# Performance work log

Hardware: AMD Instinct MI355X
Metric: run time of the kernel (lower is better)

Reference implementation:

```python
import jax, jax.numpy as jnp
import numpy as np

N_Q, M, D, DV = 4096, 32768, 512, 512  # groups, keys, key dim, value dim


def setup_inputs() -> dict:
    key = jax.random.key(0)
    k1, k2, k3 = jax.random.split(key, 3)
    query = jax.random.normal(k1, (N_Q, D), dtype=jnp.float32)
    keys = jax.random.normal(k2, (M, D), dtype=jnp.float32)
    values = jax.random.normal(k3, (M, DV), dtype=jnp.float32)
    # each query/group owns exactly M//N_Q keys -> no empty softmax rows
    tree_idx = jnp.arange(M, dtype=jnp.int32) % N_Q
    return {"query": query, "keys": keys, "values": values, "tree_idx": tree_idx}


def _l2_normalize(x, eps=1e-12):
    # matches F.normalize(x, dim=1, p=2): x / max(||x||_2, eps)
    n = jnp.linalg.norm(x, axis=1, keepdims=True)
    return x / jnp.maximum(n, eps)


def reference(query, keys, values, tree_idx):
    n_q = query.shape[0]
    # mask[q, m] = (tree_idx[m] == q); equivalent to zeros.index_add(0, tree_idx, eye(M)).bool()
    mask = tree_idx[None, :] == jnp.arange(n_q, dtype=tree_idx.dtype)[:, None]  # [N_q, M]
    query_n = _l2_normalize(query)
    keys_n = _l2_normalize(keys)
    align = query_n @ keys_n.T                      # [N_q, M] cosine similarities
    align = jnp.where(mask, align, -jnp.inf)        # masked_fill_(~mask, -inf)
    alpha = jax.nn.softmax(align, axis=1)           # segment-masked softmax per query
    att = alpha @ values                            # [N_q, DV]
    return att, alpha.sum(axis=0)
```

## Files before the change

kernel.cpp:

```cpp
#include <hip/hip_runtime.h>
#include <math.h>

#define D_DIM 512

__device__ __forceinline__ float d4(const float4& a, const float4& b) {
    return a.x*b.x + a.y*b.y + a.z*b.z + a.w*b.w;
}
__device__ __forceinline__ void fma4(float4& a, float w, const float4& v) {
    a.x += w*v.x; a.y += w*v.y; a.z += w*v.z; a.w += w*v.w;
}

__device__ __forceinline__ void g2l16(const float* g, float* l) {
    __builtin_amdgcn_global_load_lds(
        (const __attribute__((address_space(1))) void*)g,
        (__attribute__((address_space(3))) void*)l, 16, 0, 0);
}

__global__ void k_fill(const int* __restrict__ tree_idx, int m_total, int n_q,
                       int cap, int* __restrict__ cnt, int* __restrict__ keyslot) {
    const int i = blockIdx.x * blockDim.x + threadIdx.x;
    const int base = cnt[n_q];
    if (i < m_total) {
        const int q = tree_idx[i];
        const int old = atomicAdd(&cnt[q], 1);
        const int slot = (int)((unsigned)old - (unsigned)base);
        if (slot >= 0 && slot < cap) keyslot[(size_t)q * cap + slot] = i;
    }
}

__global__ __launch_bounds__(64) void attn_staged(
        const float* __restrict__ query, const float* __restrict__ keys,
        const float* __restrict__ values, const int* __restrict__ cnt,
        const int* __restrict__ keyslot, int cap,
        const int* __restrict__ tree_idx, int m_total,
        float* __restrict__ att, float* __restrict__ colsum, int n_q, int qpb) {
    extern __shared__ float smem[];
    const int lane = threadIdx.x;
    const int q0   = blockIdx.x * qpb;
    const int base = cnt[n_q];

    for (int it = 0; it < qpb; ++it) {
        const int qi = q0 + it;
        if (qi >= n_q) return;
        int nk = (int)((unsigned)cnt[qi] - (unsigned)base);
        if (nk < 0) nk = 0;
        if (nk > cap) nk = cap;
        const size_t off = (size_t)qi * cap;

        const float4* qp = (const float4*)(query + (size_t)qi * D_DIM);
        float4 qa = qp[lane], qb = qp[lane + 64];

        if (nk == 8) {
            int mv = (lane < 8) ? keyslot[off + lane] : 0;
            if (mv < 0 || mv >= m_total) mv = 0;
            int okv = (lane < 8 && tree_idx[mv] == qi) ? 1 : 0;
            int ms[8];
#pragma unroll
            for (int j = 0; j < 8; ++j) ms[j] = __shfl(mv, j);

#pragma unroll
            for (int j = 0; j < 8; ++j) {
                const float* kr = keys   + (size_t)ms[j] * D_DIM;
                const float* vr = values + (size_t)ms[j] * D_DIM;
                g2l16(kr +       (lane << 2), smem + j * 512);
                g2l16(kr + 256 + (lane << 2), smem + j * 512 + 256);
                g2l16(vr +       (lane << 2), smem + 4096 + j * 512);
                g2l16(vr + 256 + (lane << 2), smem + 4096 + j * 512 + 256);
            }
            __syncthreads();

            float pq = d4(qa, qa) + d4(qb, qb);
            float pd[8], pk[8];
#pragma unroll
            for (int j = 0; j < 8; ++j) {
                const float4* kr = (const float4*)(smem + j * 512);
                float4 ka = kr[lane], kb = kr[lane + 64];
                pd[j] = d4(qa, ka) + d4(qb, kb);
                pk[j] = d4(ka, ka) + d4(kb, kb);
            }
#pragma unroll
            for (int o = 32; o > 0; o >>= 1) {
                pq += __shfl_xor(pq, o);
#pragma unroll
                for (int j = 0; j < 8; ++j) {
                    pd[j] += __shfl_xor(pd[j], o);
                    pk[j] += __shfl_xor(pk[j], o);
                }
            }
            const float qinv = 1.0f / fmaxf(sqrtf(pq), 1e-12f);
            float e[8], sum = 0.f;
            int oks[8];
#pragma unroll
            for (int j = 0; j < 8; ++j) {
                oks[j] = __shfl(okv, j);
                e[j] = oks[j] ? __expf(pd[j] * qinv / fmaxf(sqrtf(pk[j]), 1e-12f)) : 0.f;
                sum += e[j];
            }
            const float inv = (sum > 0.f) ? 1.0f / sum : 0.f;

            float4 aa = make_float4(0.f, 0.f, 0.f, 0.f);
            float4 ab = make_float4(0.f, 0.f, 0.f, 0.f);
#pragma unroll
            for (int j = 0; j < 8; ++j) {
                const float4* vr = (const float4*)(smem + 4096 + j * 512);
                float4 va = vr[lane], vb = vr[lane + 64];
                fma4(aa, e[j], va); fma4(ab, e[j], vb);
            }
            aa.x *= inv; aa.y *= inv; aa.z *= inv; aa.w *= inv;
            ab.x *= inv; ab.y *= inv; ab.z *= inv; ab.w *= inv;
            float4* op = (float4*)(att + (size_t)qi * D_DIM);
            op[lane]      = aa;
            op[lane + 64] = ab;
            if (lane == 0) {
#pragma unroll
                for (int j = 0; j < 8; ++j)
                    if (oks[j]) colsum[ms[j]] = e[j] * inv;
            }
            __syncthreads();
        } else {
            float pq = d4(qa, qa) + d4(qb, qb);
#pragma unroll
            for (int o = 32; o > 0; o >>= 1) pq += __shfl_xor(pq, o);
            const float qinv = 1.0f / fmaxf(sqrtf(pq), 1e-12f);
            float sum = 0.f;
            float4 aa = make_float4(0.f, 0.f, 0.f, 0.f);
            float4 ab = make_float4(0.f, 0.f, 0.f, 0.f);
            for (int j = 0; j < nk; ++j) {
                int mi = keyslot[off + j];
                bool ok = (mi >= 0 && mi < m_total && tree_idx[mi] == qi);
                int ci = ok ? mi : 0;
                const float4* kp = (const float4*)(keys   + (size_t)ci * D_DIM);
                const float4* vp = (const float4*)(values + (size_t)ci * D_DIM);
                float4 ka = kp[lane], kb = kp[lane + 64];
                float pd = d4(qa, ka) + d4(qb, kb);
                float pk = d4(ka, ka) + d4(kb, kb);
#pragma unroll
                for (int o = 32; o > 0; o >>= 1) {
                    pd += __shfl_xor(pd, o);
                    pk += __shfl_xor(pk, o);
                }
                float ev = ok ? __expf(pd * qinv / fmaxf(sqrtf(pk), 1e-12f)) : 0.f;
                sum += ev;
                if (lane == 0 && ok) colsum[mi] = ev;
                float4 va = vp[lane], vb = vp[lane + 64];
                fma4(aa, ev, va); fma4(ab, ev, vb);
            }
            const float inv = (sum > 0.f) ? 1.0f / sum : 0.f;
            aa.x *= inv; aa.y *= inv; aa.z *= inv; aa.w *= inv;
            ab.x *= inv; ab.y *= inv; ab.z *= inv; ab.w *= inv;
            float4* op = (float4*)(att + (size_t)qi * D_DIM);
            op[lane]      = aa;
            op[lane + 64] = ab;
            if (lane == 0) {
                for (int j = 0; j < nk; ++j) {
                    int mi = keyslot[off + j];
                    if (mi >= 0 && mi < m_total && tree_idx[mi] == qi)
                        colsum[mi] *= inv;
                }
            }
        }
    }
}

__global__ void k_zero(int* cnt, int n) {
    int i = blockIdx.x * blockDim.x + threadIdx.x;
    if (i < n) cnt[i] = 0;
}
__global__ void k_count(const int* __restrict__ t, int* __restrict__ cnt, int m) {
    int i = blockIdx.x * blockDim.x + threadIdx.x;
    if (i < m) atomicAdd(&cnt[t[i]], 1);
}
__global__ __launch_bounds__(1024) void k_scan(int* __restrict__ cnt,
                                               int* __restrict__ offsets, int n_q) {
    __shared__ int wsum[16];
    const int tid = threadIdx.x, lane = tid & 63, wv = tid >> 6;
    const int items = (n_q + 1023) >> 10;
    const int base = tid * items;
    int local = 0;
    for (int i = 0; i < items; ++i) { int idx = base + i; if (idx < n_q) local += cnt[idx]; }
    int incl = local;
#pragma unroll
    for (int o = 1; o < 64; o <<= 1) { int v = __shfl_up(incl, o); if (lane >= o) incl += v; }
    if (lane == 63) wsum[wv] = incl;
    __syncthreads();
    if (wv == 0) {
        int v = (lane < 16) ? wsum[lane] : 0;
        int iv = v;
#pragma unroll
        for (int o = 1; o < 16; o <<= 1) { int t = __shfl_up(iv, o); if (lane >= o) iv += t; }
        if (lane < 16) wsum[lane] = iv - v;
    }
    __syncthreads();
    int run = wsum[wv] + incl - local;
    for (int i = 0; i < items; ++i) {
        int idx = base + i;
        if (idx < n_q) { int c = cnt[idx]; offsets[idx] = run; cnt[idx] = run; run += c; }
    }
    if (tid == 1023) offsets[n_q] = run;
}
__global__ void k_scatter(const int* __restrict__ t, int* __restrict__ cnt,
                          int* __restrict__ keylist, int m) {
    int i = blockIdx.x * blockDim.x + threadIdx.x;
    if (i < m) { int p = atomicAdd(&cnt[t[i]], 1); keylist[p] = i; }
}
__global__ __launch_bounds__(512, 8) void attn_fb(
        const float* __restrict__ query, const float* __restrict__ keys,
        const float* __restrict__ values, const int* __restrict__ offsets,
        const int* __restrict__ keylist, float* __restrict__ att,
        float* __restrict__ colsum) {
    __shared__ float4 s_v[8][128];
    __shared__ float  s_e[8];
    const int qi = blockIdx.x, tid = threadIdx.x, lane = tid & 63, wv = tid >> 6;
    const int off = offsets[qi];
    const int nk  = offsets[qi + 1] - off;
    const float4* qp = (const float4*)(query + (size_t)qi * D_DIM);
    float4 qa = qp[lane], qb = qp[lane + 64];
    float pq = d4(qa, qa) + d4(qb, qb);
    float4 aa = make_float4(0,0,0,0), ab = make_float4(0,0,0,0);
    float esum = 0.f;
    for (int idx = wv; idx < nk; idx += 8) {
        const int mi = keylist[off + idx];
        const float4* kp = (const float4*)(keys   + (size_t)mi * D_DIM);
        const float4* vp = (const float4*)(values + (size_t)mi * D_DIM);
        float4 ka = kp[lane], kb = kp[lane + 64];
        float4 va = vp[lane], vb = vp[lane + 64];
        float pd = d4(qa, ka) + d4(qb, kb);
        float pk = d4(ka, ka) + d4(kb, kb);
        float pq2 = pq;
#pragma unroll
        for (int o = 32; o > 0; o >>= 1) {
            pd += __shfl_xor(pd, o); pk += __shfl_xor(pk, o); pq2 += __shfl_xor(pq2, o);
        }
        const float qinv = 1.0f / fmaxf(sqrtf(pq2), 1e-12f);
        const float e = __expf(pd * qinv / fmaxf(sqrtf(pk), 1e-12f));
        esum += e;
        if (lane == 0) colsum[mi] = e;
        fma4(aa, e, va); fma4(ab, e, vb);
    }
    if (lane == 0) s_e[wv] = esum;
    s_v[wv][lane] = aa; s_v[wv][64 + lane] = ab;
    __syncthreads();
    const float tot = s_e[0]+s_e[1]+s_e[2]+s_e[3]+s_e[4]+s_e[5]+s_e[6]+s_e[7];
    const float inv = (tot > 0.f) ? 1.0f / tot : 0.f;
    if (tid < 128) {
        float4 r = s_v[0][tid];
#pragma unroll
        for (int j = 1; j < 8; ++j) { float4 p = s_v[j][tid]; r.x+=p.x; r.y+=p.y; r.z+=p.z; r.w+=p.w; }
        r.x *= inv; r.y *= inv; r.z *= inv; r.w *= inv;
        ((float4*)(att + (size_t)qi * D_DIM))[tid] = r;
    }
    if (lane == 0)
        for (int idx = wv; idx < nk; idx += 8) colsum[keylist[off + idx]] *= inv;
}

extern "C" void kernel_launch(void* const* d_in, const int* in_sizes, int n_in,
                              void* d_out, int out_size, void* d_ws, size_t ws_size,
                              hipStream_t stream) {
    const float* query    = (const float*)d_in[0];
    const float* keys     = (const float*)d_in[1];
    const float* values   = (const float*)d_in[2];
    const int*   tree_idx = (const int*)d_in[3];

    const int n_q     = in_sizes[0] / D_DIM;
    const int m_total = in_sizes[3];

    float* att    = (float*)d_out;
    float* colsum = att + (size_t)n_q * D_DIM;

    const long ws_ints = (long)(ws_size / 4);
    long cap_l = (ws_ints - (n_q + 1)) / (n_q > 0 ? n_q : 1);
    if (cap_l > 1024) cap_l = 1024;

    if (cap_l >= 8) {
        const int cap = (int)cap_l;
        int* cnt     = (int*)d_ws;
        int* keyslot = cnt + n_q + 1;
        k_fill<<<(m_total + 255) / 256, 256, 0, stream>>>(tree_idx, m_total, n_q,
                                                          cap, cnt, keyslot);
        int qpb = (n_q + 1023) / 1024;
        if (qpb < 1) qpb = 1;
        int grid = (n_q + qpb - 1) / qpb;
        attn_staged<<<grid, 64, 32768, stream>>>(query, keys, values, cnt,
                                                 keyslot, cap, tree_idx, m_total,
                                                 att, colsum, n_q, qpb);
    } else {
        int* cnt     = (int*)d_ws;
        int* offsets = cnt + n_q;
        int* keylist = offsets + n_q + 1;
        k_zero   <<<(n_q + 255) / 256, 256, 0, stream>>>(cnt, n_q);
        k_count  <<<(m_total + 255) / 256, 256, 0, stream>>>(tree_idx, cnt, m_total);
        k_scan   <<<1, 1024, 0, stream>>>(cnt, offsets, n_q);
        k_scatter<<<(m_total + 255) / 256, 256, 0, stream>>>(tree_idx, cnt, keylist, m_total);
        attn_fb  <<<n_q, 512, 0, stream>>>(query, keys, values, offsets, keylist, att, colsum);
    }
}
```

Before: 170.3 us.

## Add strided slab fast path for round-robin key-to-query assignment

k_fill now counts keys whose group differs from i % n_q. When that count is zero and the shapes fit, the attention kernel skips the keyslot indirection and the per-key tree_idx checks. It instead handles 8 queries per 256-thread block, reading the 8 keys and values of each query at fixed strided row offsets j*n_q+q, with softmax weights shared through LDS. The separate prefix-scan fallback pipeline is removed and replaced by a generic per-wave loop over keyslot. This trades gather indirection and LDS staging for a specialisation that only pays off for one input structure, though the runtime check keeps other inputs correct.

```diff
diff --git a/kernel.cpp b/kernel.cpp
--- a/kernel.cpp
+++ b/kernel.cpp
@@ -2,18 +2,13 @@
 #include <math.h>
 
 #define D_DIM 512
+#define QB 8
 
 __device__ __forceinline__ float d4(const float4& a, const float4& b) {
     return a.x*b.x + a.y*b.y + a.z*b.z + a.w*b.w;
 }
 __device__ __forceinline__ void fma4(float4& a, float w, const float4& v) {
     a.x += w*v.x; a.y += w*v.y; a.z += w*v.z; a.w += w*v.w;
-}
-
-__device__ __forceinline__ void g2l16(const float* g, float* l) {
-    __builtin_amdgcn_global_load_lds(
-        (const __attribute__((address_space(1))) void*)g,
-        (__attribute__((address_space(3))) void*)l, 16, 0, 0);
 }
 
 __global__ void k_fill(const int* __restrict__ tree_idx, int m_total, int n_q,
@@ -22,235 +17,160 @@
     const int base = cnt[n_q];
     if (i < m_total) {
         const int q = tree_idx[i];
-        const int old = atomicAdd(&cnt[q], 1);
-        const int slot = (int)((unsigned)old - (unsigned)base);
-        if (slot >= 0 && slot < cap) keyslot[(size_t)q * cap + slot] = i;
+        if (q < 0 || q >= n_q) {
+            atomicAdd(&cnt[n_q + 1], 1);
+        } else {
+            if (q != (i % n_q)) atomicAdd(&cnt[n_q + 1], 1);
+            const int old = atomicAdd(&cnt[q], 1);
+            const int slot = (int)((unsigned)old - (unsigned)base);
+            if (slot >= 0 && slot < cap) keyslot[(size_t)q * cap + slot] = i;
+        }
     }
 }
 
-__global__ __launch_bounds__(64) void attn_staged(
+__global__ void attn_slab(
         const float* __restrict__ query, const float* __restrict__ keys,
         const float* __restrict__ values, const int* __restrict__ cnt,
         const int* __restrict__ keyslot, int cap,
         const int* __restrict__ tree_idx, int m_total,
-        float* __restrict__ att, float* __restrict__ colsum, int n_q, int qpb) {
-    extern __shared__ float smem[];
-    const int lane = threadIdx.x;
-    const int q0   = blockIdx.x * qpb;
+        float* __restrict__ att, float* __restrict__ colsum,
+        int n_q, int use_slab) {
+    __shared__ float s_pq[QB];
+    __shared__ float s_pd[QB][8];
+    __shared__ float s_pk[QB][8];
+    __shared__ float s_w[QB][8];
+
+    const int q0   = blockIdx.x * QB;
     const int base = cnt[n_q];
-
-    for (int it = 0; it < qpb; ++it) {
-        const int qi = q0 + it;
-        if (qi >= n_q) return;
+    const bool slab = use_slab && (cnt[n_q + 1] == base);
+
+    if (slab) {
+        const int i  = threadIdx.x;
+        const int t  = i >> 5;
+        const int c0 = i & 31;
+        const int qrow = q0 + t;
+
+        const float4* qb = (const float4*)query + (size_t)qrow * 128 + c0;
+        float4 q4[4];
+        float pq = 0.f;
+#pragma unroll
+        for (int r = 0; r < 4; ++r) { q4[r] = qb[r * 32]; pq += d4(q4[r], q4[r]); }
+#pragma unroll
+        for (int o = 1; o < 32; o <<= 1) pq += __shfl_xor(pq, o);
+        if (c0 == 0) s_pq[t] = pq;
+
+#pragma unroll 2
+        for (int j = 0; j < 8; ++j) {
+            const float4* kb = (const float4*)keys
+                             + ((size_t)j * n_q + qrow) * 128 + c0;
+            float pd = 0.f, pk = 0.f;
+#pragma unroll
+            for (int r = 0; r < 4; ++r) {
+                float4 k4 = kb[r * 32];
+                pd += d4(q4[r], k4);
+                pk += d4(k4, k4);
+            }
+#pragma unroll
+            for (int o = 1; o < 32; o <<= 1) {
+                pd += __shfl_xor(pd, o);
+                pk += __shfl_xor(pk, o);
+            }
+            if (c0 == 0) { s_pd[t][j] = pd; s_pk[t][j] = pk; }
+        }
+        __syncthreads();
+
+        if (i < QB) {
+            const float qinv = 1.0f / fmaxf(sqrtf(s_pq[i]), 1e-12f);
+            float e[8], sum = 0.f;
+#pragma unroll
+            for (int j = 0; j < 8; ++j) {
+                e[j] = __expf(s_pd[i][j] * qinv / fmaxf(sqrtf(s_pk[i][j]), 1e-12f));
+                sum += e[j];
+            }
+            const float inv = (sum > 0.f) ? 1.0f / sum : 0.f;
+#pragma unroll
+            for (int j = 0; j < 8; ++j) {
+                const float w = e[j] * inv;
+                s_w[i][j] = w;
+                colsum[(size_t)j * n_q + q0 + i] = w;
+            }
+        }
+        __syncthreads();
+
+        float4 acc[4];
+#pragma unroll
+        for (int r = 0; r < 4; ++r) acc[r] = make_float4(0.f, 0.f, 0.f, 0.f);
+#pragma unroll 2
+        for (int j = 0; j < 8; ++j) {
+            const float w = s_w[t][j];
+            const float4* vb = (const float4*)values
+                             + ((size_t)j * n_q + qrow) * 128 + c0;
+#pragma unroll
+            for (int r = 0; r < 4; ++r) {
+                float4 v4 = vb[r * 32];
+                fma4(acc[r], w, v4);
+            }
+        }
+        float4* ob = (float4*)att + (size_t)qrow * 128 + c0;
+#pragma unroll
+        for (int r = 0; r < 4; ++r) ob[r * 32] = acc[r];
+        return;
+    }
+
+    const int lane = threadIdx.x & 63;
+    const int wv   = threadIdx.x >> 6;
+    for (int u = wv; u < QB; u += 4) {
+        const int qi = q0 + u;
+        if (qi >= n_q) continue;
         int nk = (int)((unsigned)cnt[qi] - (unsigned)base);
         if (nk < 0) nk = 0;
         if (nk > cap) nk = cap;
         const size_t off = (size_t)qi * cap;
 
         const float4* qp = (const float4*)(query + (size_t)qi * D_DIM);
-        float4 qa = qp[lane], qb = qp[lane + 64];
-
-        if (nk == 8) {
-            int mv = (lane < 8) ? keyslot[off + lane] : 0;
-            if (mv < 0 || mv >= m_total) mv = 0;
-            int okv = (lane < 8 && tree_idx[mv] == qi) ? 1 : 0;
-            int ms[8];
-#pragma unroll
-            for (int j = 0; j < 8; ++j) ms[j] = __shfl(mv, j);
-
-#pragma unroll
-            for (int j = 0; j < 8; ++j) {
-                const float* kr = keys   + (size_t)ms[j] * D_DIM;
-                const float* vr = values + (size_t)ms[j] * D_DIM;
-                g2l16(kr +       (lane << 2), smem + j * 512);
-                g2l16(kr + 256 + (lane << 2), smem + j * 512 + 256);
-                g2l16(vr +       (lane << 2), smem + 4096 + j * 512);
-                g2l16(vr + 256 + (lane << 2), smem + 4096 + j * 512 + 256);
-            }
-            __syncthreads();
-
-            float pq = d4(qa, qa) + d4(qb, qb);
-            float pd[8], pk[8];
-#pragma unroll
-            for (int j = 0; j < 8; ++j) {
-                const float4* kr = (const float4*)(smem + j * 512);
-                float4 ka = kr[lane], kb = kr[lane + 64];
-                pd[j] = d4(qa, ka) + d4(qb, kb);
-                pk[j] = d4(ka, ka) + d4(kb, kb);
-            }
+        float4 qa = qp[lane], qb2 = qp[lane + 64];
+        float pq = d4(qa, qa) + d4(qb2, qb2);
+#pragma unroll
+        for (int o = 32; o > 0; o >>= 1) pq += __shfl_xor(pq, o);
+        const float qinv = 1.0f / fmaxf(sqrtf(pq), 1e-12f);
+
+        float sum = 0.f;
+        float4 aa = make_float4(0.f, 0.f, 0.f, 0.f);
+        float4 ab = make_float4(0.f, 0.f, 0.f, 0.f);
+        for (int j = 0; j < nk; ++j) {
+            int mi = keyslot[off + j];
+            bool ok = (mi >= 0 && mi < m_total && tree_idx[mi] == qi);
+            int ci = ok ? mi : 0;
+            const float4* kp = (const float4*)(keys   + (size_t)ci * D_DIM);
+            const float4* vp = (const float4*)(values + (size_t)ci * D_DIM);
+            float4 ka = kp[lane], kb = kp[lane + 64];
+            float pd = d4(qa, ka) + d4(qb2, kb);
+            float pk = d4(ka, ka) + d4(kb, kb);
 #pragma unroll
             for (int o = 32; o > 0; o >>= 1) {
-                pq += __shfl_xor(pq, o);
-#pragma unroll
-                for (int j = 0; j < 8; ++j) {
-                    pd[j] += __shfl_xor(pd[j], o);
-                    pk[j] += __shfl_xor(pk[j], o);
-                }
-            }
-            const float qinv = 1.0f / fmaxf(sqrtf(pq), 1e-12f);
-            float e[8], sum = 0.f;
-            int oks[8];
-#pragma unroll
-            for (int j = 0; j < 8; ++j) {
-                oks[j] = __shfl(okv, j);
-                e[j] = oks[j] ? __expf(pd[j] * qinv / fmaxf(sqrtf(pk[j]), 1e-12f)) : 0.f;
-                sum += e[j];
-            }
-            const float inv = (sum > 0.f) ? 1.0f / sum : 0.f;
-
-            float4 aa = make_float4(0.f, 0.f, 0.f, 0.f);
-            float4 ab = make_float4(0.f, 0.f, 0.f, 0.f);
-#pragma unroll
-            for (int j = 0; j < 8; ++j) {
-                const float4* vr = (const float4*)(smem + 4096 + j * 512);
-                float4 va = vr[lane], vb = vr[lane + 64];
-                fma4(aa, e[j], va); fma4(ab, e[j], vb);
-            }
-            aa.x *= inv; aa.y *= inv; aa.z *= inv; aa.w *= inv;
-            ab.x *= inv; ab.y *= inv; ab.z *= inv; ab.w *= inv;
-            float4* op = (float4*)(att + (size_t)qi * D_DIM);
-            op[lane]      = aa;
-            op[lane + 64] = ab;
-            if (lane == 0) {
-#pragma unroll
-                for (int j = 0; j < 8; ++j)
-                    if (oks[j]) colsum[ms[j]] = e[j] * inv;
-            }
-            __syncthreads();
-        } else {
-            float pq = d4(qa, qa) + d4(qb, qb);
-#pragma unroll
-            for (int o = 32; o > 0; o >>= 1) pq += __shfl_xor(pq, o);
-            const float qinv = 1.0f / fmaxf(sqrtf(pq), 1e-12f);
-            float sum = 0.f;
-            float4 aa = make_float4(0.f, 0.f, 0.f, 0.f);
-            float4 ab = make_float4(0.f, 0.f, 0.f, 0.f);
+                pd += __shfl_xor(pd, o);
+                pk += __shfl_xor(pk, o);
+            }
+            float ev = ok ? __expf(pd * qinv / fmaxf(sqrtf(pk), 1e-12f)) : 0.f;
+            sum += ev;
+            if (lane == 0 && ok) colsum[mi] = ev;
+            float4 va = vp[lane], vb = vp[lane + 64];
+            fma4(aa, ev, va); fma4(ab, ev, vb);
+        }
+        const float inv = (sum > 0.f) ? 1.0f / sum : 0.f;
+        aa.x *= inv; aa.y *= inv; aa.z *= inv; aa.w *= inv;
+        ab.x *= inv; ab.y *= inv; ab.z *= inv; ab.w *= inv;
+        float4* op = (float4*)(att + (size_t)qi * D_DIM);
+        op[lane]      = aa;
+        op[lane + 64] = ab;
+        if (lane == 0) {
             for (int j = 0; j < nk; ++j) {
                 int mi = keyslot[off + j];
-                bool ok = (mi >= 0 && mi < m_total && tree_idx[mi] == qi);
-                int ci = ok ? mi : 0;
-                const float4* kp = (const float4*)(keys   + (size_t)ci * D_DIM);
-                const float4* vp = (const float4*)(values + (size_t)ci * D_DIM);
-                float4 ka = kp[lane], kb = kp[lane + 64];
-                float pd = d4(qa, ka) + d4(qb, kb);
-                float pk = d4(ka, ka) + d4(kb, kb);
-#pragma unroll
-                for (int o = 32; o > 0; o >>= 1) {
-                    pd += __shfl_xor(pd, o);
-                    pk += __shfl_xor(pk, o);
-                }
-                float ev = ok ? __expf(pd * qinv / fmaxf(sqrtf(pk), 1e-12f)) : 0.f;
-                sum += ev;
-                if (lane == 0 && ok) colsum[mi] = ev;
-                float4 va = vp[lane], vb = vp[lane + 64];
-                fma4(aa, ev, va); fma4(ab, ev, vb);
-            }
-            const float inv = (sum > 0.f) ? 1.0f / sum : 0.f;
-            aa.x *= inv; aa.y *= inv; aa.z *= inv; aa.w *= inv;
-            ab.x *= inv; ab.y *= inv; ab.z *= inv; ab.w *= inv;
-            float4* op = (float4*)(att + (size_t)qi * D_DIM);
-            op[lane]      = aa;
-            op[lane + 64] = ab;
-            if (lane == 0) {
-                for (int j = 0; j < nk; ++j) {
-                    int mi = keyslot[off + j];
-                    if (mi >= 0 && mi < m_total && tree_idx[mi] == qi)
-                        colsum[mi] *= inv;
-                }
+                if (mi >= 0 && mi < m_total && tree_idx[mi] == qi)
+                    colsum[mi] *= inv;
             }
         }
     }
-}
-
-__global__ void k_zero(int* cnt, int n) {
-    int i = blockIdx.x * blockDim.x + threadIdx.x;
-    if (i < n) cnt[i] = 0;
-}
-__global__ void k_count(const int* __restrict__ t, int* __restrict__ cnt, int m) {
-    int i = blockIdx.x * blockDim.x + threadIdx.x;
-    if (i < m) atomicAdd(&cnt[t[i]], 1);
-}
-__global__ __launch_bounds__(1024) void k_scan(int* __restrict__ cnt,
-                                               int* __restrict__ offsets, int n_q) {
-    __shared__ int wsum[16];
-    const int tid = threadIdx.x, lane = tid & 63, wv = tid >> 6;
-    const int items = (n_q + 1023) >> 10;
-    const int base = tid * items;
-    int local = 0;
-    for (int i = 0; i < items; ++i) { int idx = base + i; if (idx < n_q) local += cnt[idx]; }
-    int incl = local;
-#pragma unroll
-    for (int o = 1; o < 64; o <<= 1) { int v = __shfl_up(incl, o); if (lane >= o) incl += v; }
-    if (lane == 63) wsum[wv] = incl;
-    __syncthreads();
-    if (wv == 0) {
-        int v = (lane < 16) ? wsum[lane] : 0;
-        int iv = v;
-#pragma unroll
-        for (int o = 1; o < 16; o <<= 1) { int t = __shfl_up(iv, o); if (lane >= o) iv += t; }
-        if (lane < 16) wsum[lane] = iv - v;
-    }
-    __syncthreads();
-    int run = wsum[wv] + incl - local;
-    for (int i = 0; i < items; ++i) {
-        int idx = base + i;
-        if (idx < n_q) { int c = cnt[idx]; offsets[idx] = run; cnt[idx] = run; run += c; }
-    }
-    if (tid == 1023) offsets[n_q] = run;
-}
-__global__ void k_scatter(const int* __restrict__ t, int* __restrict__ cnt,
-                          int* __restrict__ keylist, int m) {
-    int i = blockIdx.x * blockDim.x + threadIdx.x;
-    if (i < m) { int p = atomicAdd(&cnt[t[i]], 1); keylist[p] = i; }
-}
-__global__ __launch_bounds__(512, 8) void attn_fb(
-        const float* __restrict__ query, const float* __restrict__ keys,
-        const float* __restrict__ values, const int* __restrict__ offsets,
-        const int* __restrict__ keylist, float* __restrict__ att,
-        float* __restrict__ colsum) {
-    __shared__ float4 s_v[8][128];
-    __shared__ float  s_e[8];
-    const int qi = blockIdx.x, tid = threadIdx.x, lane = tid & 63, wv = tid >> 6;
-    const int off = offsets[qi];
-    const int nk  = offsets[qi + 1] - off;
-    const float4* qp = (const float4*)(query + (size_t)qi * D_DIM);
-    float4 qa = qp[lane], qb = qp[lane + 64];
-    float pq = d4(qa, qa) + d4(qb, qb);
-    float4 aa = make_float4(0,0,0,0), ab = make_float4(0,0,0,0);
-    float esum = 0.f;
-    for (int idx = wv; idx < nk; idx += 8) {
-        const int mi = keylist[off + idx];
-        const float4* kp = (const float4*)(keys   + (size_t)mi * D_DIM);
-        const float4* vp = (const float4*)(values + (size_t)mi * D_DIM);
-        float4 ka = kp[lane], kb = kp[lane + 64];
-        float4 va = vp[lane], vb = vp[lane + 64];
-        float pd = d4(qa, ka) + d4(qb, kb);
-        float pk = d4(ka, ka) + d4(kb, kb);
-        float pq2 = pq;
-#pragma unroll
-        for (int o = 32; o > 0; o >>= 1) {
-            pd += __shfl_xor(pd, o); pk += __shfl_xor(pk, o); pq2 += __shfl_xor(pq2, o);
-        }
-        const float qinv = 1.0f / fmaxf(sqrtf(pq2), 1e-12f);
-        const float e = __expf(pd * qinv / fmaxf(sqrtf(pk), 1e-12f));
-        esum += e;
-        if (lane == 0) colsum[mi] = e;
-        fma4(aa, e, va); fma4(ab, e, vb);
-    }
-    if (lane == 0) s_e[wv] = esum;
-    s_v[wv][lane] = aa; s_v[wv][64 + lane] = ab;
-    __syncthreads();
-    const float tot = s_e[0]+s_e[1]+s_e[2]+s_e[3]+s_e[4]+s_e[5]+s_e[6]+s_e[7];
-    const float inv = (tot > 0.f) ? 1.0f / tot : 0.f;
-    if (tid < 128) {
-        float4 r = s_v[0][tid];
-#pragma unroll
-        for (int j = 1; j < 8; ++j) { float4 p = s_v[j][tid]; r.x+=p.x; r.y+=p.y; r.z+=p.z; r.w+=p.w; }
-        r.x *= inv; r.y *= inv; r.z *= inv; r.w *= inv;
-        ((float4*)(att + (size_t)qi * D_DIM))[tid] = r;
-    }
-    if (lane == 0)
-        for (int idx = wv; idx < nk; idx += 8) colsum[keylist[off + idx]] *= inv;
 }
 
 extern "C" void kernel_launch(void* const* d_in, const int* in_sizes, int n_in,
@@ -267,30 +187,20 @@
     float* att    = (float*)d_out;
     float* colsum = att + (size_t)n_q * D_DIM;
 
+    int* cnt     = (int*)d_ws;
+    int* keyslot = cnt + n_q + 2;
+
     const long ws_ints = (long)(ws_size / 4);
-    long cap_l = (ws_ints - (n_q + 1)) / (n_q > 0 ? n_q : 1);
+    long cap_l = (ws_ints - (n_q + 2)) / (n_q > 0 ? n_q : 1);
     if (cap_l > 1024) cap_l = 1024;
-
-    if (cap_l >= 8) {
-        const int cap = (int)cap_l;
-        int* cnt     = (int*)d_ws;
-        int* keyslot = cnt + n_q + 1;
-        k_fill<<<(m_total + 255) / 256, 256, 0, stream>>>(tree_idx, m_total, n_q,
-                                                          cap, cnt, keyslot);
-        int qpb = (n_q + 1023) / 1024;
-        if (qpb < 1) qpb = 1;
-        int grid = (n_q + qpb - 1) / qpb;
-        attn_staged<<<grid, 64, 32768, stream>>>(query, keys, values, cnt,
-                                                 keyslot, cap, tree_idx, m_total,
-                                                 att, colsum, n_q, qpb);
-    } else {
-        int* cnt     = (int*)d_ws;
-        int* offsets = cnt + n_q;
-        int* keylist = offsets + n_q + 1;
-        k_zero   <<<(n_q + 255) / 256, 256, 0, stream>>>(cnt, n_q);
-        k_count  <<<(m_total + 255) / 256, 256, 0, stream>>>(tree_idx, cnt, m_total);
-        k_scan   <<<1, 1024, 0, stream>>>(cnt, offsets, n_q);
-        k_scatter<<<(m_total + 255) / 256, 256, 0, stream>>>(tree_idx, cnt, keylist, m_total);
-        attn_fb  <<<n_q, 512, 0, stream>>>(query, keys, values, offsets, keylist, att, colsum);
-    }
-}
+    int cap = (cap_l >= 8) ? (int)cap_l : 8;
+
+    const int use_slab = (n_q > 0) && (n_q % QB == 0) && (m_total == 8 * n_q);
+
+    k_fill<<<(m_total + 255) / 256, 256, 0, stream>>>(tree_idx, m_total, n_q,
+                                                      cap, cnt, keyslot);
+    const int grid = (n_q + QB - 1) / QB;
+    attn_slab<<<grid, 256, 0, stream>>>(query, keys, values, cnt, keyslot, cap,
+                                        tree_idx, m_total, att, colsum,
+                                        n_q, use_slab);
+}
```

New measurement: 158.6 us. -6.9%, faster.
